# Optimization experiments

Measured on AMD Instinct MI355X. Metric: run time of the kernel, lower is better.

Reference implementation:

```python
import jax, jax.numpy as jnp
import numpy as np

NUM_M = 2_000_000
NUM_T = 512
N = 16
NUM_GEN = N * (N - 1) // 2  # 120
NUM_STEPS = 64
TAU = 1.0


def _make_bases():
    # skew-symmetric so(n) basis, matching the torch buffer construction order
    bases = np.zeros((NUM_GEN, N, N), np.float32)
    k = 0
    for i in range(N):
        for j in range(i + 1, N):
            bases[k, i, j] = -1.0
            bases[k, j, i] = 1.0
            k += 1
    return jnp.asarray(bases)


def setup_inputs() -> dict:
    key = jax.random.key(0)
    ks = jax.random.split(key, 8)
    W = jax.random.normal(ks[0], (NUM_M, N), jnp.float32)
    emb_weight = W / jnp.linalg.norm(W, axis=-1, keepdims=True)  # normalized at init
    transition_coeffs = jax.random.normal(ks[1], (NUM_T, NUM_GEN), jnp.float32) * 0.1

    def lin(k, fi, fo):  # torch nn.Linear default init
        bound = 1.0 / np.sqrt(fi)
        kw, kb = jax.random.split(k)
        w = jax.random.uniform(kw, (fi, fo), jnp.float32, -bound, bound)
        b = jax.random.uniform(kb, (fo,), jnp.float32, -bound, bound)
        return w, b

    w1, b1 = lin(ks[2], 2 * N, 256)
    w2, b2 = lin(ks[3], 256, 128)
    w3, b3 = lin(ks[4], 128, NUM_T)

    v_src = jax.random.uniform(ks[5], (1, NUM_M), jnp.float32)
    v_target = jax.random.uniform(ks[6], (1, NUM_M), jnp.float32)
    # pre-sampled Gumbel(0,1) noise for gumbel_softmax, one draw per step
    u = jax.random.uniform(ks[7], (NUM_STEPS, 1, NUM_T), jnp.float32, 1e-6, 1.0 - 1e-6)
    gumbel = -jnp.log(-jnp.log(u))

    return {
        'v_src': v_src, 'v_target': v_target,
        'emb_weight': emb_weight, 'transition_coeffs': transition_coeffs,
        'bases': _make_bases(),
        'w1': w1, 'b1': b1, 'w2': w2, 'b2': b2, 'w3': w3, 'b3': b3,
        'gumbel': gumbel, 'num_steps': NUM_STEPS,
    }


def reference(v_src, v_target, emb_weight, transition_coeffs, bases,
              w1, b1, w2, b2, w3, b3, gumbel, num_steps):
    # training=True path of PetriNetAlignmentPredictor.forward, tau=1.0
    embs = emb_weight / jnp.linalg.norm(emb_weight, axis=-1, keepdims=True)
    v_cur = v_src @ embs      # [1, n]  (memory-bound matvec over num_m)
    v_tgt = v_target @ embs   # [1, n]
    gens = jnp.einsum('tg,gnm->tnm', transition_coeffs, bases)  # [num_t, n, n]
    expm_b = jax.vmap(jax.scipy.linalg.expm)

    def step(v, g):
        h = jax.nn.relu(jnp.concatenate([v, v_tgt], axis=-1) @ w1 + b1)
        h = jax.nn.relu(h @ w2 + b2)
        logits = h @ w3 + b3                       # [1, num_t]
        # gumbel_softmax(hard=True) with straight-through estimator
        y = jax.nn.softmax((logits + g) / TAU, axis=-1)
        hard = jax.nn.one_hot(jnp.argmax(y, axis=-1), logits.shape[-1], dtype=y.dtype)
        one_hot = hard + y - jax.lax.stop_gradient(y)
        omega = jnp.einsum('bt,tnm->bnm', one_hot, gens)  # skew-symmetric [1, n, n]
        R = expm_b(omega)
        v2 = jnp.einsum('bnm,bm->bn', R, v)
        v2 = v2 / jnp.linalg.norm(v2, axis=-1, keepdims=True)
        return v2, logits

    v_fin, logits_seq = jax.lax.scan(step, v_cur, gumbel[:num_steps])
    pred_marking = jax.nn.softmax(v_fin @ embs.T, axis=-1)  # [1, num_m]
    return pred_marking, logits_seq[:, 0, :]  # squeeze batch dim -> [num_steps, num_t]
```

## Files before the change

### kernel.cpp

```cpp
#include <hip/hip_runtime.h>

#define M_TOTAL   2000000
#define NT        512
#define K1_BLOCKS 1024
#define K3_BLOCKS 2048

__device__ __forceinline__ float rlf(float v, int l) {
    union { float f; int i; } u; u.f = v;
    u.i = __builtin_amdgcn_readlane(u.i, l);
    return u.f;
}

__device__ __forceinline__ void bar_lds() {
    asm volatile("s_waitcnt lgkmcnt(0)" ::: "memory");
    __builtin_amdgcn_s_barrier();
    asm volatile("" ::: "memory");
}

#define DPPMAXU(m, ctrl) { unsigned _d = (unsigned)__builtin_amdgcn_update_dpp(0, (int)(m), (ctrl), 0xF, 0xF, true); \
                           if (_d > (m)) (m) = _d; }
#define DPPADDF(s, ctrl) { float _d = __int_as_float(__builtin_amdgcn_update_dpp(0, __float_as_int(s), (ctrl), 0xF, 0xF, true)); \
                           (s) += _d; }

__device__ __forceinline__ unsigned orderf(float f) {
    unsigned u = __float_as_uint(f);
    return u ^ (((unsigned)((int)u >> 31)) | 0x80000000u);
}

__device__ __forceinline__ uint2 pick2(uint2 a, uint2 b) {
    bool takeb = (b.x > a.x) || (b.x == a.x && b.y < a.y);
    return takeb ? b : a;
}

#define REP16(M)  M(0) M(1) M(2) M(3) M(4) M(5) M(6) M(7) M(8) M(9) M(10) M(11) M(12) M(13) M(14) M(15)
#define REP16B(M) M(16) M(17) M(18) M(19) M(20) M(21) M(22) M(23) M(24) M(25) M(26) M(27) M(28) M(29) M(30) M(31)

#define VLD4(dst, base, c) { const volatile float* _p = (base) + 4*(c); \
    dst.x = _p[0]; dst.y = _p[1]; dst.z = _p[2]; dst.w = _p[3]; }

extern "C" __global__ __launch_bounds__(256)
void k_reduce(const float* __restrict__ emb, const float* __restrict__ vsrc,
              const float* __restrict__ vtgt, double* __restrict__ partials)
{
    const int tid = threadIdx.x;
    const int bid = blockIdx.x;
    double aS[4], aT[4];
#pragma unroll
    for (int i = 0; i < 4; i++) { aS[i] = 0.0; aT[i] = 0.0; }

    const float4* emb4 = (const float4*)emb;
    for (long long f = (long long)bid * 256 + tid; f < (long long)M_TOTAL * 4;
         f += (long long)K1_BLOCKS * 256) {
        float4 e = emb4[f];
        long long r = f >> 2;
        float sq = fmaf(e.x, e.x, fmaf(e.y, e.y, fmaf(e.z, e.z, e.w * e.w)));
        sq += __shfl_xor(sq, 1);
        sq += __shfl_xor(sq, 2);
        float invn = 1.0f / sqrtf(sq);
        float s = vsrc[r] * invn;
        float t = vtgt[r] * invn;
        aS[0] += (double)(s * e.x); aS[1] += (double)(s * e.y);
        aS[2] += (double)(s * e.z); aS[3] += (double)(s * e.w);
        aT[0] += (double)(t * e.x); aT[1] += (double)(t * e.y);
        aT[2] += (double)(t * e.z); aT[3] += (double)(t * e.w);
    }
#pragma unroll
    for (int i = 0; i < 4; i++) {
#pragma unroll
        for (int off = 32; off >= 4; off >>= 1) {
            aS[i] += __shfl_down(aS[i], off);
            aT[i] += __shfl_down(aT[i], off);
        }
    }
    __shared__ double lred[4][32];
    int lane = tid & 63, wv = tid >> 6;
    if (lane < 4) {
#pragma unroll
        for (int i = 0; i < 4; i++) {
            lred[wv][lane * 4 + i]      = aS[i];
            lred[wv][16 + lane * 4 + i] = aT[i];
        }
    }
    __syncthreads();
    if (tid < 32) {
        double v = lred[0][tid] + lred[1][tid] + lred[2][tid] + lred[3][tid];
        partials[(long long)bid * 32 + tid] = v;
    }
}

extern "C" __global__ __launch_bounds__(256)
void k_pre(const float* __restrict__ tc, float* __restrict__ Rtab,
           const float* __restrict__ w2g, const float* __restrict__ w3g,
           float* __restrict__ w2R, float* __restrict__ w3R,
           double* __restrict__ totalp)
{
    const int bid = blockIdx.x;
    const int t = threadIdx.x;

    if (bid < 512) {
        const int i = t >> 4, j = t & 15;
        __shared__ float Om[256];
        __shared__ float Ms[256];

        const float* crow = tc + bid * 120;
        float o = 0.0f;
        if (i < j)      o = -crow[(i * (31 - i)) / 2 + (j - i - 1)];
        else if (i > j) o =  crow[(j * (31 - j)) / 2 + (i - j - 1)];
        Om[t] = o;
        Ms[t] = o;
        float s = (i == j ? 1.0f : 0.0f) + o;
        __syncthreads();

#pragma unroll
        for (int k = 2; k <= 16; k++) {
            float a0 = 0.0f, a1 = 0.0f, a2 = 0.0f, a3 = 0.0f;
#pragma unroll
            for (int m = 0; m < 4; m++) {
                a0 = fmaf(Om[i * 16 + m],      Ms[m * 16 + j],        a0);
                a1 = fmaf(Om[i * 16 + 4 + m],  Ms[(4 + m) * 16 + j],  a1);
                a2 = fmaf(Om[i * 16 + 8 + m],  Ms[(8 + m) * 16 + j],  a2);
                a3 = fmaf(Om[i * 16 + 12 + m], Ms[(12 + m) * 16 + j], a3);
            }
            float acc = ((a0 + a1) + (a2 + a3)) * (1.0f / (float)k);
            __syncthreads();
            Ms[t] = acc;
            s += acc;
            __syncthreads();
        }
        Rtab[bid * 256 + t] = s;
    } else {
        if (bid == 512 && t == 0) totalp[0] = 0.0;
        if (t >= 128) return;
        const int b = bid - 512;
        const int k = t;
        if (b < 512) {
            w3R[b * 128 + k] = w3g[k * 512 + b];
        } else {
            const int p2 = b - 512;
            const int j2 = k;
            for (int m = 0; m < 64; m++)
                w2R[(((p2 << 7) | j2) * 64) + m] = w2g[(64 * p2 + m) * 128 + j2];
        }
    }
}

extern "C" __global__ __launch_bounds__(512)
__attribute__((amdgpu_waves_per_eu(2, 2)))
void k_steps(const double* __restrict__ partials,
             const float* __restrict__ w1g, const float* __restrict__ b1g,
             const float* __restrict__ b2g, const float* __restrict__ b3g,
             const float* __restrict__ w2R, const float* __restrict__ w3R,
             const float* __restrict__ Rtab, const float* __restrict__ gum,
             const int* __restrict__ nsp,
             float* __restrict__ outL, float* __restrict__ vf_out)
{
    __shared__ __align__(16) float h1s[256];
    __shared__ __align__(16) float h2p[512];
    __shared__ __align__(16) float h2s[128];
    __shared__ float xs[32];
    __shared__ float b2s[128];
    __shared__ uint2 kidx[8];
    __shared__ double dred[512];

    const int t = threadIdx.x;
    const int lane = t & 63;
    const int wv = t >> 6;
    const int j2 = t & 127, p2 = t >> 7;
    const int c1 = t & 255;

    const volatile float* w3v = (const volatile float*)(w3R + (size_t)t * 128);
    const volatile float* w2v = (const volatile float*)(w2R + (size_t)t * 64);
#define W3D(c) float4 w3_##c; VLD4(w3_##c, w3v, c)
    REP16(W3D) REP16B(W3D)
#undef W3D
#define W2D(c) float4 w2_##c; VLD4(w2_##c, w2v, c)
    REP16(W2D)
#undef W2D
    const float b3r = b3g[t];

    float w1r[16];
    {
        const volatile float* w1v = (const volatile float*)w1g;
#pragma unroll
        for (int m = 0; m < 16; m++) w1r[m] = w1v[m * 256 + c1];
    }
    if (t < 128) b2s[t] = b2g[t];

    float warm = 0.0f;
    for (int i = t; i < 512 * 256 / 4; i += 512) {
        float4 rv = ((const float4*)Rtab)[i];
        warm += (rv.x + rv.y) + (rv.z + rv.w);
    }

    {
        double v = 0.0;
#pragma unroll 4
        for (int i = 0; i < (K1_BLOCKS * 32) / 512; i++) v += partials[i * 512 + t];
        dred[t] = v;
    }

    int ns = nsp[0];
    if (ns > 64) ns = 64;
    if (ns < 0)  ns = 0;
    if (ns == -2147483647) vf_out[0] = warm;

    __syncthreads();
    if (t < 32) {
        double s = 0.0;
#pragma unroll
        for (int j = 0; j < 16; j++) s += dred[t + 32 * j];
        xs[t] = (float)s;
    }
    __syncthreads();

    float b1e = 0.0f, vreg = 0.0f;
    if (t < 256) {
        float a = b1g[c1];
#pragma unroll
        for (int m = 0; m < 16; m++)
            a = fmaf(xs[16 + m], w1g[(16 + m) * 256 + c1], a);
        b1e = a;
        vreg = xs[lane & 15];
    }

    if (ns == 0 && t < 16) vf_out[t] = xs[t];

    for (int step = 0; step < ns; step++) {
        float gv = gum[step * 512 + t];

        if (t < 256) {
            float a0 = 0.0f, a1 = 0.0f;
#pragma unroll
            for (int m = 0; m < 8; m++) {
                a0 = fmaf(rlf(vreg, m),     w1r[m],     a0);
                a1 = fmaf(rlf(vreg, 8 + m), w1r[8 + m], a1);
            }
            h1s[t] = fmaxf((a0 + a1) + b1e, 0.0f);
        }
        bar_lds();

        {
            const float2* h1b = (const float2*)&h1s[p2 << 6];
            float a0 = 0.0f, a1 = 0.0f, a2 = 0.0f, a3 = 0.0f;
#define L2C(c) { float2 mA = h1b[2*(c)]; float2 mB = h1b[2*(c)+1]; \
                 a0 = fmaf(mA.x, w2_##c.x, a0); \
                 a1 = fmaf(mA.y, w2_##c.y, a1); \
                 a2 = fmaf(mB.x, w2_##c.z, a2); \
                 a3 = fmaf(mB.y, w2_##c.w, a3); }
            REP16(L2C)
#undef L2C
            h2p[(p2 << 7) | j2] = (a0 + a1) + (a2 + a3);
        }
        bar_lds();

        if (t < 128) {
            float s = ((h2p[t] + h2p[128 + t]) + (h2p[256 + t] + h2p[384 + t])) + b2s[t];
            h2s[t] = fmaxf(s, 0.0f);
        }
        bar_lds();

        float lg;
        {
            const float2* h2b = (const float2*)h2s;
            float lg0 = 0.0f, lg1 = 0.0f, lg2 = 0.0f, lg3 = 0.0f;
#define L3C(c) { float2 mA = h2b[2*(c)]; float2 mB = h2b[2*(c)+1]; \
                 lg0 = fmaf(mA.x, w3_##c.x, lg0); \
                 lg1 = fmaf(mA.y, w3_##c.y, lg1); \
                 lg2 = fmaf(mB.x, w3_##c.z, lg2); \
                 lg3 = fmaf(mB.y, w3_##c.w, lg3); }
            REP16(L3C) REP16B(L3C)
#undef L3C
            lg = ((lg0 + lg1) + (lg2 + lg3)) + b3r;
        }
        outL[step * 512 + t] = lg;

        {
            unsigned ok = orderf(lg + gv);
            unsigned m = ok;
            DPPMAXU(m, 0x111)
            DPPMAXU(m, 0x112)
            DPPMAXU(m, 0x114)
            DPPMAXU(m, 0x118)
            DPPMAXU(m, 0x142)
            DPPMAXU(m, 0x143)
            unsigned wmax = (unsigned)__builtin_amdgcn_readlane((int)m, 63);
            unsigned long long mask = __ballot(ok == wmax);
            if (lane == 0) {
                uint2 kv; kv.x = wmax; kv.y = (unsigned)(wv * 64 + (__ffsll(mask) - 1));
                kidx[wv] = kv;
            }
        }
        bar_lds();

        if (t < 256 && lane < 16) {
            uint2 K0, K1, K2, K3, K4, K5, K6, K7;
            { uint4 a = *(const uint4*)&kidx[0]; K0.x=a.x; K0.y=a.y; K1.x=a.z; K1.y=a.w; }
            { uint4 a = *(const uint4*)&kidx[2]; K2.x=a.x; K2.y=a.y; K3.x=a.z; K3.y=a.w; }
            { uint4 a = *(const uint4*)&kidx[4]; K4.x=a.x; K4.y=a.y; K5.x=a.z; K5.y=a.w; }
            { uint4 a = *(const uint4*)&kidx[6]; K6.x=a.x; K6.y=a.y; K7.x=a.z; K7.y=a.w; }
            uint2 w01 = pick2(K0, K1), w23 = pick2(K2, K3);
            uint2 w45 = pick2(K4, K5), w67 = pick2(K6, K7);
            uint2 win = pick2(pick2(w01, w23), pick2(w45, w67));
            const int bi = (int)win.y;

            const float4* rp = (const float4*)(Rtab + (size_t)bi * 256 + lane * 16);
            float4 ra = rp[0], rb = rp[1], rc = rp[2], rd = rp[3];
            float p0 = ra.x * rlf(vreg, 0);
            float p1 = rb.x * rlf(vreg, 4);
            float p2r = rc.x * rlf(vreg, 8);
            float p3 = rd.x * rlf(vreg, 12);
            p0 = fmaf(ra.y, rlf(vreg, 1), p0);
            p1 = fmaf(rb.y, rlf(vreg, 5), p1);
            p2r = fmaf(rc.y, rlf(vreg, 9), p2r);
            p3 = fmaf(rd.y, rlf(vreg, 13), p3);
            p0 = fmaf(ra.z, rlf(vreg, 2), p0);
            p1 = fmaf(rb.z, rlf(vreg, 6), p1);
            p2r = fmaf(rc.z, rlf(vreg, 10), p2r);
            p3 = fmaf(rd.z, rlf(vreg, 14), p3);
            p0 = fmaf(ra.w, rlf(vreg, 3), p0);
            p1 = fmaf(rb.w, rlf(vreg, 7), p1);
            p2r = fmaf(rc.w, rlf(vreg, 11), p2r);
            p3 = fmaf(rd.w, rlf(vreg, 15), p3);
            float pr = (p0 + p1) + (p2r + p3);

            float s2 = pr * pr;
            DPPADDF(s2, 0x111)
            DPPADDF(s2, 0x112)
            DPPADDF(s2, 0x114)
            DPPADDF(s2, 0x118)
            float n2 = rlf(s2, 15);
            float invn = 1.0f / sqrtf(n2);
            vreg = pr * invn;
            if (step == ns - 1 && t < 16) vf_out[t] = vreg;
        }
    }
}

extern "C" __global__ __launch_bounds__(256)
void k_scores(const float* __restrict__ emb, const float* __restrict__ vf16,
              float* __restrict__ outP, double* __restrict__ totalp)
{
    __shared__ float vfs[16];
    const int tid = threadIdx.x;
    const int bid = blockIdx.x;
    const int q = tid & 3;
    if (tid < 16) vfs[tid] = vf16[tid];
    __syncthreads();
    float v0 = vfs[q * 4 + 0], v1 = vfs[q * 4 + 1], v2 = vfs[q * 4 + 2], v3 = vfs[q * 4 + 3];

    const float4* emb4 = (const float4*)emb;
    double bsum = 0.0;
    for (long long f = (long long)bid * 256 + tid; f < (long long)M_TOTAL * 4;
         f += (long long)K3_BLOCKS * 256) {
        float4 e = emb4[f];
        long long r = f >> 2;
        float sq = fmaf(e.x, e.x, fmaf(e.y, e.y, fmaf(e.z, e.z, e.w * e.w)));
        float d  = fmaf(e.x, v0, fmaf(e.y, v1, fmaf(e.z, v2, e.w * v3)));
        sq += __shfl_xor(sq, 1);  d += __shfl_xor(d, 1);
        sq += __shfl_xor(sq, 2);  d += __shfl_xor(d, 2);
        float ex = expf(d / sqrtf(sq));
        if (q == 0) {
            outP[r] = ex;
            bsum += (double)ex;
        }
    }
#pragma unroll
    for (int off = 4; off <= 32; off <<= 1) bsum += __shfl_down(bsum, off);
    __shared__ double lred[4];
    if ((tid & 63) == 0) lred[tid >> 6] = bsum;
    __syncthreads();
    if (tid == 0) atomicAdd(totalp, lred[0] + lred[1] + lred[2] + lred[3]);
}

extern "C" __global__ __launch_bounds__(256)
void k_scale(float* __restrict__ outP, const double* __restrict__ totalp)
{
    const float inv = 1.0f / (float)totalp[0];
    long long r4 = (long long)blockIdx.x * 256 + threadIdx.x;
    if (r4 < M_TOTAL / 4) {
        float4* p = (float4*)outP;
        float4 v = p[r4];
        v.x *= inv; v.y *= inv; v.z *= inv; v.w *= inv;
        p[r4] = v;
    }
}

extern "C" void kernel_launch(void* const* d_in, const int* in_sizes, int n_in,
                              void* d_out, int out_size, void* d_ws, size_t ws_size,
                              hipStream_t stream)
{
    const float* vsrc = (const float*)d_in[0];
    const float* vtgt = (const float*)d_in[1];
    const float* emb  = (const float*)d_in[2];
    const float* tc   = (const float*)d_in[3];
    const float* w1 = (const float*)d_in[5];
    const float* b1 = (const float*)d_in[6];
    const float* w2 = (const float*)d_in[7];
    const float* b2 = (const float*)d_in[8];
    const float* w3 = (const float*)d_in[9];
    const float* b3 = (const float*)d_in[10];
    const float* gum = (const float*)d_in[11];
    const int* nsp   = (const int*)d_in[12];

    float* outP = (float*)d_out;
    float* outL = outP + M_TOTAL;

    double* wsd      = (double*)d_ws;
    double* partials = wsd;
    double* totalp   = wsd + 2048 * 32;
    float*  vf       = (float*)(totalp + 1);

    float* Rtab = outP;
    float* w3R  = outP + 131072;
    float* w2R  = outP + 196608;

    k_pre<<<1028, 256, 0, stream>>>(tc, Rtab, w2, w3, w2R, w3R, totalp);
    k_reduce<<<K1_BLOCKS, 256, 0, stream>>>(emb, vsrc, vtgt, partials);
    k_steps<<<1, 512, 0, stream>>>(partials, w1, b1, b2, b3, w2R, w3R, Rtab, gum, nsp, outL, vf);
    k_scores<<<K3_BLOCKS, 256, 0, stream>>>(emb, vf, outP, totalp);
    k_scale<<<(M_TOTAL / 4 + 255) / 256, 256, 0, stream>>>(outP, totalp);
}
```

Before: 569.7 us.

## Split layer-2 across quad lanes with DPP reduction, move w1 to LDS, swap shuffles for DPP

Layer 2 of the per-step MLP is now split so that each group of 4 lanes covers one output column, and the partial sums are combined with quad DPP adds. This removes the h2p partial buffer and one barrier per step. The w2 reorder in k_pre is rewritten to match the interleaved layout, and w1 moves from registers into LDS to free VGPRs. Layer-2 and layer-3 LDS loads are software-pipelined in chunks, and quad shuffles in the reduce and score kernels are replaced with DPP quad-perm adds. The trade-off is extra LDS traffic for w1 in exchange for fewer barriers and register relief in the serial single-block step kernel.

```diff
diff --git a/kernel.cpp b/kernel.cpp
--- a/kernel.cpp
+++ b/kernel.cpp
@@ -21,6 +21,8 @@
                            if (_d > (m)) (m) = _d; }
 #define DPPADDF(s, ctrl) { float _d = __int_as_float(__builtin_amdgcn_update_dpp(0, __float_as_int(s), (ctrl), 0xF, 0xF, true)); \
                            (s) += _d; }
+#define QP_XOR1 0xB1
+#define QP_XOR2 0x4E
 
 __device__ __forceinline__ unsigned orderf(float f) {
     unsigned u = __float_as_uint(f);
@@ -54,8 +56,8 @@
         float4 e = emb4[f];
         long long r = f >> 2;
         float sq = fmaf(e.x, e.x, fmaf(e.y, e.y, fmaf(e.z, e.z, e.w * e.w)));
-        sq += __shfl_xor(sq, 1);
-        sq += __shfl_xor(sq, 2);
+        DPPADDF(sq, QP_XOR1)
+        DPPADDF(sq, QP_XOR2)
         float invn = 1.0f / sqrtf(sq);
         float s = vsrc[r] * invn;
         float t = vtgt[r] * invn;
@@ -130,16 +132,13 @@
         Rtab[bid * 256 + t] = s;
     } else {
         if (bid == 512 && t == 0) totalp[0] = 0.0;
-        if (t >= 128) return;
-        const int b = bid - 512;
-        const int k = t;
-        if (b < 512) {
-            w3R[b * 128 + k] = w3g[k * 512 + b];
-        } else {
-            const int p2 = b - 512;
-            const int j2 = k;
-            for (int m = 0; m < 64; m++)
-                w2R[(((p2 << 7) | j2) * 64) + m] = w2g[(64 * p2 + m) * 128 + j2];
+        const int tt = bid - 512;
+        if (t < 128) {
+            w3R[tt * 128 + t] = w3g[t * 512 + tt];
+        } else if (t < 192) {
+            const int q = t - 128;
+            const int kk = 2 * (tt & 3) + 8 * (q >> 1) + (q & 1);
+            w2R[tt * 64 + q] = w2g[kk * 128 + (tt >> 2)];
         }
     }
 }
@@ -154,8 +153,8 @@
              const int* __restrict__ nsp,
              float* __restrict__ outL, float* __restrict__ vf_out)
 {
+    __shared__ __align__(16) float w1s[16 * 256];
     __shared__ __align__(16) float h1s[256];
-    __shared__ __align__(16) float h2p[512];
     __shared__ __align__(16) float h2s[128];
     __shared__ float xs[32];
     __shared__ float b2s[128];
@@ -165,7 +164,7 @@
     const int t = threadIdx.x;
     const int lane = t & 63;
     const int wv = t >> 6;
-    const int j2 = t & 127, p2 = t >> 7;
+    const int c4 = t & 3;
     const int c1 = t & 255;
 
     const volatile float* w3v = (const volatile float*)(w3R + (size_t)t * 128);
@@ -178,12 +177,7 @@
 #undef W2D
     const float b3r = b3g[t];
 
-    float w1r[16];
-    {
-        const volatile float* w1v = (const volatile float*)w1g;
-#pragma unroll
-        for (int m = 0; m < 16; m++) w1r[m] = w1v[m * 256 + c1];
-    }
+    for (int i = t; i < 16 * 256; i += 512) w1s[i] = w1g[i];
     if (t < 128) b2s[t] = b2g[t];
 
     float warm = 0.0f;
@@ -232,30 +226,46 @@
             float a0 = 0.0f, a1 = 0.0f;
 #pragma unroll
             for (int m = 0; m < 8; m++) {
-                a0 = fmaf(rlf(vreg, m),     w1r[m],     a0);
-                a1 = fmaf(rlf(vreg, 8 + m), w1r[8 + m], a1);
+                a0 = fmaf(rlf(vreg, m),     w1s[m * 256 + t],       a0);
+                a1 = fmaf(rlf(vreg, 8 + m), w1s[(8 + m) * 256 + t], a1);
             }
             h1s[t] = fmaxf((a0 + a1) + b1e, 0.0f);
         }
         bar_lds();
 
         {
-            const float2* h1b = (const float2*)&h1s[p2 << 6];
+            const float2* h1b = (const float2*)h1s;
             float a0 = 0.0f, a1 = 0.0f, a2 = 0.0f, a3 = 0.0f;
-#define L2C(c) { float2 mA = h1b[2*(c)]; float2 mB = h1b[2*(c)+1]; \
-                 a0 = fmaf(mA.x, w2_##c.x, a0); \
-                 a1 = fmaf(mA.y, w2_##c.y, a1); \
-                 a2 = fmaf(mB.x, w2_##c.z, a2); \
-                 a3 = fmaf(mB.y, w2_##c.w, a3); }
-            REP16(L2C)
-#undef L2C
-            h2p[(p2 << 7) | j2] = (a0 + a1) + (a2 + a3);
-        }
-        bar_lds();
-
-        if (t < 128) {
-            float s = ((h2p[t] + h2p[128 + t]) + (h2p[256 + t] + h2p[384 + t])) + b2s[t];
-            h2s[t] = fmaxf(s, 0.0f);
+            float2 nA0, nA1, nA2, nA3, nA4, nA5, nA6, nA7;
+            float2 nB0, nB1, nB2, nB3, nB4, nB5, nB6, nB7;
+#define L2LD(R, ch) \
+            (R##0) = h1b[c4 + 32*(ch) +  0]; (R##1) = h1b[c4 + 32*(ch) +  4]; \
+            (R##2) = h1b[c4 + 32*(ch) +  8]; (R##3) = h1b[c4 + 32*(ch) + 12]; \
+            (R##4) = h1b[c4 + 32*(ch) + 16]; (R##5) = h1b[c4 + 32*(ch) + 20]; \
+            (R##6) = h1b[c4 + 32*(ch) + 24]; (R##7) = h1b[c4 + 32*(ch) + 28];
+#define L2CH(R, W0, W1, Wa, Wb) \
+            a0 = fmaf((R##0).x, W0.x, a0); a1 = fmaf((R##0).y, W0.y, a1); \
+            a2 = fmaf((R##1).x, W0.z, a2); a3 = fmaf((R##1).y, W0.w, a3); \
+            a0 = fmaf((R##2).x, W1.x, a0); a1 = fmaf((R##2).y, W1.y, a1); \
+            a2 = fmaf((R##3).x, W1.z, a2); a3 = fmaf((R##3).y, W1.w, a3); \
+            a0 = fmaf((R##4).x, Wa.x, a0); a1 = fmaf((R##4).y, Wa.y, a1); \
+            a2 = fmaf((R##5).x, Wa.z, a2); a3 = fmaf((R##5).y, Wa.w, a3); \
+            a0 = fmaf((R##6).x, Wb.x, a0); a1 = fmaf((R##6).y, Wb.y, a1); \
+            a2 = fmaf((R##7).x, Wb.z, a2); a3 = fmaf((R##7).y, Wb.w, a3);
+            L2LD(nA, 0)
+            L2LD(nB, 1)
+            L2CH(nA, w2_0,  w2_1,  w2_2,  w2_3)
+            L2LD(nA, 2)
+            L2CH(nB, w2_4,  w2_5,  w2_6,  w2_7)
+            L2LD(nB, 3)
+            L2CH(nA, w2_8,  w2_9,  w2_10, w2_11)
+            L2CH(nB, w2_12, w2_13, w2_14, w2_15)
+#undef L2LD
+#undef L2CH
+            float asum = (a0 + a1) + (a2 + a3);
+            DPPADDF(asum, QP_XOR1)
+            DPPADDF(asum, QP_XOR2)
+            if (c4 == 0) h2s[t >> 2] = fmaxf(asum + b2s[t >> 2], 0.0f);
         }
         bar_lds();
 
@@ -263,13 +273,40 @@
         {
             const float2* h2b = (const float2*)h2s;
             float lg0 = 0.0f, lg1 = 0.0f, lg2 = 0.0f, lg3 = 0.0f;
-#define L3C(c) { float2 mA = h2b[2*(c)]; float2 mB = h2b[2*(c)+1]; \
-                 lg0 = fmaf(mA.x, w3_##c.x, lg0); \
-                 lg1 = fmaf(mA.y, w3_##c.y, lg1); \
-                 lg2 = fmaf(mB.x, w3_##c.z, lg2); \
-                 lg3 = fmaf(mB.y, w3_##c.w, lg3); }
-            REP16(L3C) REP16B(L3C)
-#undef L3C
+            float2 mA0, mA1, mA2, mA3, mA4, mA5, mA6, mA7;
+            float2 mB0, mB1, mB2, mB3, mB4, mB5, mB6, mB7;
+#define L3LD(R, ch) \
+            (R##0) = h2b[8*(ch) + 0]; (R##1) = h2b[8*(ch) + 1]; \
+            (R##2) = h2b[8*(ch) + 2]; (R##3) = h2b[8*(ch) + 3]; \
+            (R##4) = h2b[8*(ch) + 4]; (R##5) = h2b[8*(ch) + 5]; \
+            (R##6) = h2b[8*(ch) + 6]; (R##7) = h2b[8*(ch) + 7];
+#define L3CH(R, W0, W1, Wa, Wb) \
+            lg0 = fmaf((R##0).x, W0.x, lg0); lg1 = fmaf((R##0).y, W0.y, lg1); \
+            lg2 = fmaf((R##1).x, W0.z, lg2); lg3 = fmaf((R##1).y, W0.w, lg3); \
+            lg0 = fmaf((R##2).x, W1.x, lg0); lg1 = fmaf((R##2).y, W1.y, lg1); \
+            lg2 = fmaf((R##3).x, W1.z, lg2); lg3 = fmaf((R##3).y, W1.w, lg3); \
+            lg0 = fmaf((R##4).x, Wa.x, lg0); lg1 = fmaf((R##4).y, Wa.y, lg1); \
+            lg2 = fmaf((R##5).x, Wa.z, lg2); lg3 = fmaf((R##5).y, Wa.w, lg3); \
+            lg0 = fmaf((R##6).x, Wb.x, lg0); lg1 = fmaf((R##6).y, Wb.y, lg1); \
+            lg2 = fmaf((R##7).x, Wb.z, lg2); lg3 = fmaf((R##7).y, Wb.w, lg3);
+            L3LD(mA, 0)
+            L3LD(mB, 1)
+            L3CH(mA, w3_0,  w3_1,  w3_2,  w3_3)
+            L3LD(mA, 2)
+            L3CH(mB, w3_4,  w3_5,  w3_6,  w3_7)
+            L3LD(mB, 3)
+            L3CH(mA, w3_8,  w3_9,  w3_10, w3_11)
+            L3LD(mA, 4)
+            L3CH(mB, w3_12, w3_13, w3_14, w3_15)
+            L3LD(mB, 5)
+            L3CH(mA, w3_16, w3_17, w3_18, w3_19)
+            L3LD(mA, 6)
+            L3CH(mB, w3_20, w3_21, w3_22, w3_23)
+            L3LD(mB, 7)
+            L3CH(mA, w3_24, w3_25, w3_26, w3_27)
+            L3CH(mB, w3_28, w3_29, w3_30, w3_31)
+#undef L3LD
+#undef L3CH
             lg = ((lg0 + lg1) + (lg2 + lg3)) + b3r;
         }
         outL[step * 512 + t] = lg;
@@ -356,8 +393,10 @@
         long long r = f >> 2;
         float sq = fmaf(e.x, e.x, fmaf(e.y, e.y, fmaf(e.z, e.z, e.w * e.w)));
         float d  = fmaf(e.x, v0, fmaf(e.y, v1, fmaf(e.z, v2, e.w * v3)));
-        sq += __shfl_xor(sq, 1);  d += __shfl_xor(d, 1);
-        sq += __shfl_xor(sq, 2);  d += __shfl_xor(d, 2);
+        DPPADDF(sq, QP_XOR1)
+        DPPADDF(d,  QP_XOR1)
+        DPPADDF(sq, QP_XOR2)
+        DPPADDF(d,  QP_XOR2)
         float ex = expf(d / sqrtf(sq));
         if (q == 0) {
             outP[r] = ex;
@@ -414,7 +453,7 @@
     float* w3R  = outP + 131072;
     float* w2R  = outP + 196608;
 
-    k_pre<<<1028, 256, 0, stream>>>(tc, Rtab, w2, w3, w2R, w3R, totalp);
+    k_pre<<<1024, 256, 0, stream>>>(tc, Rtab, w2, w3, w2R, w3R, totalp);
     k_reduce<<<K1_BLOCKS, 256, 0, stream>>>(emb, vsrc, vtgt, partials);
     k_steps<<<1, 512, 0, stream>>>(partials, w1, b1, b2, b3, w2R, w3R, Rtab, gum, nsp, outL, vf);
     k_scores<<<K3_BLOCKS, 256, 0, stream>>>(emb, vf, outP, totalp);
```

Measured after the change: 648.3 us. 13.8% more time.
